# Kernel tuning notes

Measured on AMD Instinct MI355X. Metric: run time of the kernel, lower is better.

## Reference

```python
import jax, jax.numpy as jnp
import numpy as np

B, T, C = 8, 1024, 768
H, D = 12, 64

def setup_inputs() -> dict:
    key = jax.random.key(0)
    ks = jax.random.split(key, 6)
    s = 0.02
    return {
        "x": jax.random.normal(ks[0], (B, T, C), dtype=jnp.float32),
        "Wq": jax.random.normal(ks[1], (H, C, D), dtype=jnp.float32) * s,
        "Wk": jax.random.normal(ks[2], (H, C, D), dtype=jnp.float32) * s,
        "Wv": jax.random.normal(ks[3], (H, C, D), dtype=jnp.float32) * s,
        "Wproj": jax.random.normal(ks[4], (C, C), dtype=jnp.float32) * s,
        "bproj": jnp.zeros((C,), dtype=jnp.float32),
    }

def reference(x, Wq, Wk, Wv, Wproj, bproj):
    # per-head projections, vectorized over heads: [B,H,T,D]
    q = jnp.einsum('btc,hcd->bhtd', x, Wq)
    k = jnp.einsum('btc,hcd->bhtd', x, Wk)
    v = jnp.einsum('btc,hcd->bhtd', x, Wv)
    scale = 1.0 / jnp.sqrt(jnp.asarray(q.shape[-1], q.dtype))
    scores = jnp.einsum('bhtd,bhsd->bhts', q, k) * scale  # [B,H,T,T]
    attn = jax.nn.softmax(scores, axis=-1)
    out = jnp.einsum('bhts,bhsd->bhtd', attn, v)          # [B,H,T,D]
    # concat heads along last dim -> [B,T,H*D]
    out = out.transpose(0, 2, 1, 3).reshape(x.shape[0], x.shape[1], -1)
    return out @ Wproj + bproj
```

## Files before the change

### kernel.cpp

```cpp
#include <hip/hip_runtime.h>
#include <hip/hip_bf16.h>

using u16 = unsigned short;

typedef __attribute__((ext_vector_type(8))) short bf16x8;
typedef __attribute__((ext_vector_type(4))) float f32x4;
typedef __attribute__((ext_vector_type(16))) float f32x16;

#define B_ 8
#define T_ 1024
#define C_ 768
#define H_ 12
#define D_ 64

typedef const void __attribute__((address_space(1))) gv_t;
typedef void __attribute__((address_space(3))) lv_t;

__device__ __forceinline__ void gload_lds16(const void* g, void* l) {
  __builtin_amdgcn_global_load_lds((gv_t*)g, (lv_t*)l, 16, 0, 0);
}

__device__ __forceinline__ u16 f2b(float f) {
  union { float f; unsigned u; } a; a.f = f;
  unsigned r = a.u + 0x7FFFu + ((a.u >> 16) & 1u);
  return (u16)(r >> 16);
}

__device__ __forceinline__ float fexp2(float x) {
  float r;
  asm("v_exp_f32 %0, %1" : "=v"(r) : "v"(x));
  return r;
}

__device__ __forceinline__ unsigned cvtpk_bf16(float lo, float hi) {
  unsigned r;
  asm("v_cvt_pk_bf16_f32 %0, %1, %2" : "=v"(r) : "v"(lo), "v"(hi));
  return r;
}
__device__ __forceinline__ void plane32_swap(unsigned &a, unsigned &b) {
  asm volatile("v_permlane32_swap_b32 %0, %1" : "+v"(a), "+v"(b));
}

__global__ __launch_bounds__(256) void prep_all(
    const float* __restrict__ x,
    const float* __restrict__ Wq, const float* __restrict__ Wk,
    const float* __restrict__ Wv, const float* __restrict__ Wp,
    u16* __restrict__ Xb, u16* __restrict__ Wqkvt, u16* __restrict__ Wpt)
{
  int bb = blockIdx.x;
  if (bb < 3072) {
    int i = (bb * 256 + threadIdx.x) * 8;
    float4 a = *(const float4*)(x + i);
    float4 b = *(const float4*)(x + i + 4);
    union { bf16x8 v; u16 s[8]; } o;
    o.s[0] = f2b(a.x); o.s[1] = f2b(a.y); o.s[2] = f2b(a.z); o.s[3] = f2b(a.w);
    o.s[4] = f2b(b.x); o.s[5] = f2b(b.y); o.s[6] = f2b(b.z); o.s[7] = f2b(b.w);
    *(bf16x8*)(Xb + i) = o.v;
  } else {
    int idx = (bb - 3072) * 256 + threadIdx.x;
    int p = idx / 147456;
    int r = idx - p * 147456;
    if (p < 3) {
      const float* W = (p == 0) ? Wq : ((p == 1) ? Wk : Wv);
      int d4 = r & 15;
      int c  = (r >> 4) % 768;
      int h  = r / 12288;
      float4 v = *(const float4*)(W + (size_t)h * 49152 + (size_t)c * 64 + d4 * 4);
      size_t nb = (size_t)p * 589824 + ((size_t)h * 64 + d4 * 4) * 768 + c;
      Wqkvt[nb]           = f2b(v.x);
      Wqkvt[nb + 768]     = f2b(v.y);
      Wqkvt[nb + 1536]    = f2b(v.z);
      Wqkvt[nb + 2304]    = f2b(v.w);
    } else {
      int co4 = r % 192;
      int ci  = r / 192;
      float4 v = *(const float4*)(Wp + (size_t)ci * 768 + co4 * 4);
      size_t ob = (size_t)(co4 * 4) * 768 + ci;
      Wpt[ob]        = f2b(v.x);
      Wpt[ob + 768]  = f2b(v.y);
      Wpt[ob + 1536] = f2b(v.z);
      Wpt[ob + 2304] = f2b(v.w);
    }
  }
}

__global__ __launch_bounds__(512) void gemm_qkv(
    const u16* __restrict__ X, const u16* __restrict__ Wt,
    u16* __restrict__ Qw, u16* __restrict__ Kw, u16* __restrict__ Vt)
{
  __shared__ __align__(16) u16 As[256 * 64];
  __shared__ __align__(16) u16 Bs[128 * 64];
  const int t = threadIdx.x;
  const int l = t & 63, w = t >> 6;
  const int lr = l & 15;
  const int hc = (l >> 4) * 16;
  const int m0 = blockIdx.x * 256;
  const int n0 = blockIdx.y * 128;
  const int wr = (w >> 1) * 64;
  const int wc = (w & 1) * 64;

  f32x4 acc[4][4] = {};

  for (int k0 = 0; k0 < 768; k0 += 64) {
    #pragma unroll
    for (int q = 0; q < 4; ++q) {
      int db = q * 8192 + t * 16;
      int row = db >> 7;
      int cb = (db ^ ((row & 7) << 4)) & 127;
      gload_lds16((const char*)X + ((size_t)(m0 + row) * 768 + k0) * 2 + cb,
                  (char*)As + db);
    }
    #pragma unroll
    for (int q = 0; q < 2; ++q) {
      int db = q * 8192 + t * 16;
      int row = db >> 7;
      int cb = (db ^ ((row & 7) << 4)) & 127;
      gload_lds16((const char*)Wt + ((size_t)(n0 + row) * 768 + k0) * 2 + cb,
                  (char*)Bs + db);
    }
    asm volatile("s_waitcnt vmcnt(0)" ::: "memory");
    __syncthreads();
    #pragma unroll
    for (int kq = 0; kq < 2; ++kq) {
      bf16x8 af[4], bfr[4];
      #pragma unroll
      for (int i = 0; i < 4; ++i) {
        int ra = wr + i * 16 + lr;
        int Ua = ra * 128 + kq * 64 + hc;
        af[i] = *(const bf16x8*)((const char*)As + (Ua ^ ((ra & 7) << 4)));
        int rb = wc + i * 16 + lr;
        int Ub = rb * 128 + kq * 64 + hc;
        bfr[i] = *(const bf16x8*)((const char*)Bs + (Ub ^ ((rb & 7) << 4)));
      }
      #pragma unroll
      for (int i = 0; i < 4; ++i)
        #pragma unroll
        for (int j = 0; j < 4; ++j)
          acc[i][j] = __builtin_amdgcn_mfma_f32_16x16x32_bf16(af[i], bfr[j],
                                                              acc[i][j], 0, 0, 0);
    }
    __syncthreads();
  }

  #pragma unroll
  for (int j = 0; j < 4; ++j) {
    int col_g = n0 + wc + j * 16 + lr;
    int p = (col_g >= 1536) ? 2 : ((col_g >= 768) ? 1 : 0);
    int rr = col_g - p * 768;
    int h = rr >> 6, d = rr & 63;
    #pragma unroll
    for (int i = 0; i < 4; ++i) {
      int rg0 = m0 + wr + i * 16 + ((l >> 4) << 2);
      int b = rg0 >> 10, tt = rg0 & 1023;
      if (p == 0) {
        size_t base = (((size_t)b * H_ + h) * T_ + tt) * D_ + d;
        #pragma unroll
        for (int r = 0; r < 4; ++r)
          Qw[base + (size_t)r * D_] = f2b(acc[i][j][r] * 0.18033688f);
      } else if (p == 1) {
        size_t base = (((size_t)b * H_ + h) * T_ + tt) * D_ + d;
        #pragma unroll
        for (int r = 0; r < 4; ++r) Kw[base + (size_t)r * D_] = f2b(acc[i][j][r]);
      } else {
        unsigned long long pk =
            (unsigned long long)f2b(acc[i][j][0]) |
            ((unsigned long long)f2b(acc[i][j][1]) << 16) |
            ((unsigned long long)f2b(acc[i][j][2]) << 32) |
            ((unsigned long long)f2b(acc[i][j][3]) << 48);
        *reinterpret_cast<unsigned long long*>(
            &Vt[(((size_t)b * H_ + h) * D_ + d) * T_ + tt]) = pk;
      }
    }
  }
}

__global__ __launch_bounds__(256) void gemm_proj(
    const u16* __restrict__ A, const u16* __restrict__ Wt,
    const float* __restrict__ bias, float* __restrict__ O)
{
  __shared__ __align__(16) u16 As[128 * 64];
  __shared__ __align__(16) u16 Bs[128 * 64];
  const int t = threadIdx.x;
  const int l = t & 63, w = t >> 6;
  const int lr = l & 15;
  const int hc = (l >> 4) * 16;
  const int m0 = blockIdx.x * 128;
  const int n0 = blockIdx.y * 128;
  const int wr = (w >> 1) * 64, wc = (w & 1) * 64;

  f32x4 acc[4][4] = {};
  for (int k0 = 0; k0 < 768; k0 += 64) {
    #pragma unroll
    for (int q = 0; q < 4; ++q) {
      int db = q * 4096 + t * 16;
      int row = db >> 7;
      int cb = (db ^ ((row & 7) << 4)) & 127;
      gload_lds16((const char*)A + ((size_t)(m0 + row) * 768 + k0) * 2 + cb,
                  (char*)As + db);
      gload_lds16((const char*)Wt + ((size_t)(n0 + row) * 768 + k0) * 2 + cb,
                  (char*)Bs + db);
    }
    asm volatile("s_waitcnt vmcnt(0)" ::: "memory");
    __syncthreads();
    #pragma unroll
    for (int kq = 0; kq < 2; ++kq) {
      bf16x8 af[4], bfr[4];
      #pragma unroll
      for (int i = 0; i < 4; ++i) {
        int ra = wr + i * 16 + lr;
        int Ua = ra * 128 + kq * 64 + hc;
        af[i] = *(const bf16x8*)((const char*)As + (Ua ^ ((ra & 7) << 4)));
        int rb = wc + i * 16 + lr;
        int Ub = rb * 128 + kq * 64 + hc;
        bfr[i] = *(const bf16x8*)((const char*)Bs + (Ub ^ ((rb & 7) << 4)));
      }
      #pragma unroll
      for (int i = 0; i < 4; ++i)
        #pragma unroll
        for (int j = 0; j < 4; ++j)
          acc[i][j] = __builtin_amdgcn_mfma_f32_16x16x32_bf16(af[i], bfr[j],
                                                              acc[i][j], 0, 0, 0);
    }
    __syncthreads();
  }

  #pragma unroll
  for (int j = 0; j < 4; ++j) {
    int col_g = n0 + wc + j * 16 + lr;
    float bb = bias[col_g];
    #pragma unroll
    for (int i = 0; i < 4; ++i) {
      int rg0 = m0 + wr + i * 16 + ((l >> 4) << 2);
      #pragma unroll
      for (int r = 0; r < 4; ++r)
        O[(size_t)(rg0 + r) * C_ + col_g] = acc[i][j][r] + bb;
    }
  }
}

__global__ __launch_bounds__(256) void attn_fwd(
    const u16* __restrict__ Qw, const u16* __restrict__ Kw,
    const u16* __restrict__ VT, u16* __restrict__ AO)
{
  __shared__ __align__(16) u16 Ks[2][64 * 64];
  __shared__ __align__(16) u16 Vs[3][64 * 64];
  const int t = threadIdx.x, l = t & 63;
  const int lq = l & 31, lh = l >> 5;

  const int bid = blockIdx.x;
  const int bh = (bid & 7) * 12 + ((bid >> 3) >> 3);
  const int qt = (bid >> 3) & 7;
  const int b = bh / H_, h = bh - b * H_;
  const u16* Qh = Qw + (size_t)bh * (T_ * D_);
  const char* Kp = (const char*)(Kw + (size_t)bh * (T_ * D_));
  const char* Vp = (const char*)(VT + (size_t)bh * (D_ * T_));
  const int q0w = qt * 128 + (t >> 6) * 32;
  const int qrow = q0w + lq;

  bf16x8 qf[4];
  #pragma unroll
  for (int ks = 0; ks < 4; ++ks)
    qf[ks] = *(const bf16x8*)(Qh + (size_t)qrow * D_ + lh * 8 + ks * 16);

  bf16x8 ones;
  {
    union { u16 s[8]; bf16x8 v; } u;
    #pragma unroll
    for (int j = 0; j < 8; ++j) u.s[j] = 0x3F80;
    ones = u.v;
  }

  f32x16 oA = {}, oB = {}, lacc = {};
  bf16x8 pbP[4];

  const int db0 = t * 16, db1 = 4096 + t * 16;
  const int row0 = db0 >> 7, row1 = db1 >> 7;
  const int cb0 = (db0 ^ ((row0 & 7) << 4)) & 127;
  const int cb1 = (db1 ^ ((row1 & 7) << 4)) & 127;

#define ISSUE_TILE(KT, KB, VB)                                                   \
  gload_lds16(Kp + (size_t)((KT) + row0) * 128 + cb0, (char*)Ks[KB] + db0);      \
  gload_lds16(Kp + (size_t)((KT) + row1) * 128 + cb1, (char*)Ks[KB] + db1);      \
  gload_lds16(Vp + (size_t)row0 * 2048 + (KT) * 2 + cb0, (char*)Vs[VB] + db0);   \
  gload_lds16(Vp + (size_t)row1 * 2048 + (KT) * 2 + cb1, (char*)Vs[VB] + db1);

  ISSUE_TILE(0, 0, 0)

  int wv = 1, pv = 2;

  for (int kt_i = 0; kt_i < 16; ++kt_i) {
    const int cur = kt_i & 1;
    asm volatile("s_waitcnt vmcnt(0)" ::: "memory");
    __syncthreads();
    if (kt_i < 15) { ISSUE_TILE((kt_i + 1) * 64, cur ^ 1, wv) }

    f32x16 sA = {}, sB = {};
    {
      bf16x8 ka[4];
      #pragma unroll
      for (int ks = 0; ks < 4; ++ks) {
        int row = lq;
        int U = row * 128 + ks * 32 + lh * 16;
        ka[ks] = *(const bf16x8*)((const char*)Ks[cur] + (U ^ ((row & 7) << 4)));
      }
      #pragma unroll
      for (int ks = 0; ks < 4; ++ks)
        sA = __builtin_amdgcn_mfma_f32_32x32x16_bf16(ka[ks], qf[ks], sA, 0, 0, 0);
      #pragma unroll
      for (int ks = 0; ks < 4; ++ks) {
        int row = lq + 32;
        int U = row * 128 + ks * 32 + lh * 16;
        ka[ks] = *(const bf16x8*)((const char*)Ks[cur] + (U ^ ((row & 7) << 4)));
      }
      #pragma unroll
      for (int ks = 0; ks < 4; ++ks)
        sB = __builtin_amdgcn_mfma_f32_32x32x16_bf16(ka[ks], qf[ks], sB, 0, 0, 0);
    }

    if (kt_i > 0) {
      const char* Vb = (const char*)Vs[pv];
      bf16x8 va[4];
      #pragma unroll
      for (int ks = 0; ks < 4; ++ks) {
        int row = lq;
        int U = row * 128 + ks * 32 + lh * 16;
        va[ks] = *(const bf16x8*)(Vb + (U ^ ((row & 7) << 4)));
      }
      #pragma unroll
      for (int ks = 0; ks < 4; ++ks)
        oA = __builtin_amdgcn_mfma_f32_32x32x16_bf16(va[ks], pbP[ks], oA, 0, 0, 0);
      #pragma unroll
      for (int ks = 0; ks < 4; ++ks) {
        int row = lq + 32;
        int U = row * 128 + ks * 32 + lh * 16;
        va[ks] = *(const bf16x8*)(Vb + (U ^ ((row & 7) << 4)));
      }
      #pragma unroll
      for (int ks = 0; ks < 4; ++ks)
        oB = __builtin_amdgcn_mfma_f32_32x32x16_bf16(va[ks], pbP[ks], oB, 0, 0, 0);
      #pragma unroll
      for (int ks = 0; ks < 4; ++ks)
        lacc = __builtin_amdgcn_mfma_f32_32x32x16_bf16(ones, pbP[ks], lacc, 0, 0, 0);
    }

    #pragma unroll
    for (int r = 0; r < 16; ++r) {
      sA[r] = fexp2(sA[r]);
      sB[r] = fexp2(sB[r]);
    }

    #pragma unroll
    for (int ks = 0; ks < 4; ++ks) {
      f32x16& S = (ks < 2) ? sA : sB;
      const int g = (ks & 1) * 8;
      unsigned a0 = cvtpk_bf16(S[g + 0], S[g + 1]);
      unsigned a1 = cvtpk_bf16(S[g + 2], S[g + 3]);
      unsigned b0 = cvtpk_bf16(S[g + 4], S[g + 5]);
      unsigned b1 = cvtpk_bf16(S[g + 6], S[g + 7]);
      plane32_swap(a0, b0);
      plane32_swap(a1, b1);
      union { unsigned wd[4]; bf16x8 v; } u;
      u.wd[0] = a0; u.wd[1] = a1; u.wd[2] = b0; u.wd[3] = b1;
      pbP[ks] = u.v;
    }

    wv = (wv == 2) ? 0 : wv + 1;
    pv = (pv == 2) ? 0 : pv + 1;
  }
#undef ISSUE_TILE

  {
    const char* Vb = (const char*)Vs[pv];
    bf16x8 va[4];
    #pragma unroll
    for (int ks = 0; ks < 4; ++ks) {
      int row = lq;
      int U = row * 128 + ks * 32 + lh * 16;
      va[ks] = *(const bf16x8*)(Vb + (U ^ ((row & 7) << 4)));
    }
    #pragma unroll
    for (int ks = 0; ks < 4; ++ks)
      oA = __builtin_amdgcn_mfma_f32_32x32x16_bf16(va[ks], pbP[ks], oA, 0, 0, 0);
    #pragma unroll
    for (int ks = 0; ks < 4; ++ks) {
      int row = lq + 32;
      int U = row * 128 + ks * 32 + lh * 16;
      va[ks] = *(const bf16x8*)(Vb + (U ^ ((row & 7) << 4)));
    }
    #pragma unroll
    for (int ks = 0; ks < 4; ++ks)
      oB = __builtin_amdgcn_mfma_f32_32x32x16_bf16(va[ks], pbP[ks], oB, 0, 0, 0);
    #pragma unroll
    for (int ks = 0; ks < 4; ++ks)
      lacc = __builtin_amdgcn_mfma_f32_32x32x16_bf16(ones, pbP[ks], lacc, 0, 0, 0);
  }

  float inv = 1.0f / lacc[0];
  size_t base = ((size_t)b * T_ + qrow) * C_ + h * D_;
  #pragma unroll
  for (int dh = 0; dh < 2; ++dh) {
    const f32x16& OO = dh ? oB : oA;
    #pragma unroll
    for (int g = 0; g < 4; ++g) {
      int d0 = 8 * g + 4 * lh + 32 * dh;
      unsigned long long pk =
          (unsigned long long)f2b(OO[4 * g + 0] * inv) |
          ((unsigned long long)f2b(OO[4 * g + 1] * inv) << 16) |
          ((unsigned long long)f2b(OO[4 * g + 2] * inv) << 32) |
          ((unsigned long long)f2b(OO[4 * g + 3] * inv) << 48);
      *reinterpret_cast<unsigned long long*>(&AO[base + d0]) = pk;
    }
  }
}

extern "C" void kernel_launch(void* const* d_in, const int* in_sizes, int n_in,
                              void* d_out, int out_size, void* d_ws, size_t ws_size,
                              hipStream_t stream) {
  (void)in_sizes; (void)n_in; (void)out_size;
  const float* x     = (const float*)d_in[0];
  const float* Wq    = (const float*)d_in[1];
  const float* Wk    = (const float*)d_in[2];
  const float* Wv    = (const float*)d_in[3];
  const float* Wproj = (const float*)d_in[4];
  const float* bproj = (const float*)d_in[5];

  const size_t NEEDED = 55050240;
  if (ws_size < NEEDED) return;

  char* ws = (char*)d_ws;
  u16* Wpt   = (u16*)(ws);
  u16* Qw    = (u16*)(ws + 1179648);
  u16* Kw    = (u16*)(ws + 13762560);
  u16* Vt    = (u16*)(ws + 26345472);
  u16* Xb    = (u16*)(ws + 38928384);
  u16* AO    = (u16*)(ws + 38928384);
  u16* Wqkvt = (u16*)(ws + 51511296);

  prep_all<<<dim3(5376), dim3(256), 0, stream>>>(x, Wq, Wk, Wv, Wproj, Xb, Wqkvt, Wpt);
  gemm_qkv<<<dim3(32, 18), dim3(512), 0, stream>>>(Xb, Wqkvt, Qw, Kw, Vt);
  attn_fwd<<<dim3(768), dim3(256), 0, stream>>>(Qw, Kw, Vt, AO);
  gemm_proj<<<dim3(64, 6), dim3(256), 0, stream>>>(AO, Wpt, bproj, (float*)d_out);
}
```

Before: 127.9 us.

## Double-buffer LDS tiles in QKV GEMM to overlap global loads with MFMA

The QKV projection GEMM now keeps two LDS buffers for the A and B tiles. It issues the next k-tile's global-to-LDS loads, split across the two k-halves, while MFMAs run on the current buffer, and it drops the trailing barrier. This aims to hide global load latency behind compute. In exchange, LDS use doubles to 96KB per block, which may limit occupancy, and only one barrier per iteration now guards buffer reuse.

```diff
diff --git a/kernel.cpp b/kernel.cpp
--- a/kernel.cpp
+++ b/kernel.cpp
@@ -88,8 +88,8 @@
     const u16* __restrict__ X, const u16* __restrict__ Wt,
     u16* __restrict__ Qw, u16* __restrict__ Kw, u16* __restrict__ Vt)
 {
-  __shared__ __align__(16) u16 As[256 * 64];
-  __shared__ __align__(16) u16 Bs[128 * 64];
+  __shared__ __align__(16) u16 As[2][256 * 64];
+  __shared__ __align__(16) u16 Bs[2][128 * 64];
   const int t = threadIdx.x;
   const int l = t & 63, w = t >> 6;
   const int lr = l & 15;
@@ -99,38 +99,45 @@
   const int wr = (w >> 1) * 64;
   const int wc = (w & 1) * 64;
 
+#define QKV_ISSUE_A(K0, BUF)                                                    \
+  _Pragma("unroll")                                                             \
+  for (int q = 0; q < 4; ++q) {                                                 \
+    int db = q * 8192 + t * 16;                                                 \
+    int row = db >> 7;                                                          \
+    int cb = (db ^ ((row & 7) << 4)) & 127;                                     \
+    gload_lds16((const char*)X + ((size_t)(m0 + row) * 768 + (K0)) * 2 + cb,    \
+                (char*)As[BUF] + db);                                           \
+  }
+#define QKV_ISSUE_B(K0, BUF)                                                    \
+  _Pragma("unroll")                                                             \
+  for (int q = 0; q < 2; ++q) {                                                 \
+    int db = q * 8192 + t * 16;                                                 \
+    int row = db >> 7;                                                          \
+    int cb = (db ^ ((row & 7) << 4)) & 127;                                     \
+    gload_lds16((const char*)Wt + ((size_t)(n0 + row) * 768 + (K0)) * 2 + cb,   \
+                (char*)Bs[BUF] + db);                                           \
+  }
+
+  QKV_ISSUE_A(0, 0)
+  QKV_ISSUE_B(0, 0)
+
   f32x4 acc[4][4] = {};
-
-  for (int k0 = 0; k0 < 768; k0 += 64) {
-    #pragma unroll
-    for (int q = 0; q < 4; ++q) {
-      int db = q * 8192 + t * 16;
-      int row = db >> 7;
-      int cb = (db ^ ((row & 7) << 4)) & 127;
-      gload_lds16((const char*)X + ((size_t)(m0 + row) * 768 + k0) * 2 + cb,
-                  (char*)As + db);
-    }
-    #pragma unroll
-    for (int q = 0; q < 2; ++q) {
-      int db = q * 8192 + t * 16;
-      int row = db >> 7;
-      int cb = (db ^ ((row & 7) << 4)) & 127;
-      gload_lds16((const char*)Wt + ((size_t)(n0 + row) * 768 + k0) * 2 + cb,
-                  (char*)Bs + db);
-    }
+  for (int it = 0; it < 12; ++it) {
+    const int c = it & 1;
     asm volatile("s_waitcnt vmcnt(0)" ::: "memory");
     __syncthreads();
-    #pragma unroll
-    for (int kq = 0; kq < 2; ++kq) {
+    if (it < 11) { QKV_ISSUE_A((it + 1) * 64, c ^ 1) }
+
+    {
       bf16x8 af[4], bfr[4];
       #pragma unroll
       for (int i = 0; i < 4; ++i) {
         int ra = wr + i * 16 + lr;
-        int Ua = ra * 128 + kq * 64 + hc;
-        af[i] = *(const bf16x8*)((const char*)As + (Ua ^ ((ra & 7) << 4)));
+        int Ua = ra * 128 + hc;
+        af[i] = *(const bf16x8*)((const char*)As[c] + (Ua ^ ((ra & 7) << 4)));
         int rb = wc + i * 16 + lr;
-        int Ub = rb * 128 + kq * 64 + hc;
-        bfr[i] = *(const bf16x8*)((const char*)Bs + (Ub ^ ((rb & 7) << 4)));
+        int Ub = rb * 128 + hc;
+        bfr[i] = *(const bf16x8*)((const char*)Bs[c] + (Ub ^ ((rb & 7) << 4)));
       }
       #pragma unroll
       for (int i = 0; i < 4; ++i)
@@ -139,8 +146,30 @@
           acc[i][j] = __builtin_amdgcn_mfma_f32_16x16x32_bf16(af[i], bfr[j],
                                                               acc[i][j], 0, 0, 0);
     }
-    __syncthreads();
-  }
+
+    if (it < 11) { QKV_ISSUE_B((it + 1) * 64, c ^ 1) }
+
+    {
+      bf16x8 af[4], bfr[4];
+      #pragma unroll
+      for (int i = 0; i < 4; ++i) {
+        int ra = wr + i * 16 + lr;
+        int Ua = ra * 128 + 64 + hc;
+        af[i] = *(const bf16x8*)((const char*)As[c] + (Ua ^ ((ra & 7) << 4)));
+        int rb = wc + i * 16 + lr;
+        int Ub = rb * 128 + 64 + hc;
+        bfr[i] = *(const bf16x8*)((const char*)Bs[c] + (Ub ^ ((rb & 7) << 4)));
+      }
+      #pragma unroll
+      for (int i = 0; i < 4; ++i)
+        #pragma unroll
+        for (int j = 0; j < 4; ++j)
+          acc[i][j] = __builtin_amdgcn_mfma_f32_16x16x32_bf16(af[i], bfr[j],
+                                                              acc[i][j], 0, 0, 0);
+    }
+  }
+#undef QKV_ISSUE_A
+#undef QKV_ISSUE_B
 
   #pragma unroll
   for (int j = 0; j < 4; ++j) {
```

After: 138.3 us. +8.1%, slower.

## Replace LDS-tiled GEMMs with per-wave direct-global-load MFMA tiles

Applied to the files above, without the earlier changes.

Both the QKV and output-projection GEMMs drop shared-memory staging and block-wide barriers. Each wave now computes its own 64x64 output tile and loads the MFMA operands straight from global memory (through L2/L1) into registers. This removes the LDS round trip and the syncthreads stalls and raises occupancy, but gives up cross-wave data reuse in LDS and issues uncoalesced, strided 16-byte loads with no software prefetch, so the GEMMs depend on cache hit rates.

```diff
diff --git a/kernel.cpp b/kernel.cpp
--- a/kernel.cpp
+++ b/kernel.cpp
@@ -84,73 +84,49 @@
   }
 }
 
-__global__ __launch_bounds__(512) void gemm_qkv(
+__global__ __launch_bounds__(256, 4) void gemm_qkv(
     const u16* __restrict__ X, const u16* __restrict__ Wt,
     u16* __restrict__ Qw, u16* __restrict__ Kw, u16* __restrict__ Vt)
 {
-  __shared__ __align__(16) u16 As[256 * 64];
-  __shared__ __align__(16) u16 Bs[128 * 64];
   const int t = threadIdx.x;
   const int l = t & 63, w = t >> 6;
   const int lr = l & 15;
-  const int hc = (l >> 4) * 16;
-  const int m0 = blockIdx.x * 256;
-  const int n0 = blockIdx.y * 128;
-  const int wr = (w >> 1) * 64;
-  const int wc = (w & 1) * 64;
+  const int ko = (l >> 4) * 8;
+  const int gw = blockIdx.x * 4 + w;
+  const int mw = gw / 36, nw = gw - mw * 36;
+  const int m0 = mw * 64, n0 = nw * 64;
+
+  const u16* Xa = X  + (size_t)(m0 + lr) * 768 + ko;
+  const u16* Wa = Wt + (size_t)(n0 + lr) * 768 + ko;
 
   f32x4 acc[4][4] = {};
-
-  for (int k0 = 0; k0 < 768; k0 += 64) {
-    #pragma unroll
-    for (int q = 0; q < 4; ++q) {
-      int db = q * 8192 + t * 16;
-      int row = db >> 7;
-      int cb = (db ^ ((row & 7) << 4)) & 127;
-      gload_lds16((const char*)X + ((size_t)(m0 + row) * 768 + k0) * 2 + cb,
-                  (char*)As + db);
-    }
-    #pragma unroll
-    for (int q = 0; q < 2; ++q) {
-      int db = q * 8192 + t * 16;
-      int row = db >> 7;
-      int cb = (db ^ ((row & 7) << 4)) & 127;
-      gload_lds16((const char*)Wt + ((size_t)(n0 + row) * 768 + k0) * 2 + cb,
-                  (char*)Bs + db);
-    }
-    asm volatile("s_waitcnt vmcnt(0)" ::: "memory");
-    __syncthreads();
-    #pragma unroll
-    for (int kq = 0; kq < 2; ++kq) {
-      bf16x8 af[4], bfr[4];
-      #pragma unroll
-      for (int i = 0; i < 4; ++i) {
-        int ra = wr + i * 16 + lr;
-        int Ua = ra * 128 + kq * 64 + hc;
-        af[i] = *(const bf16x8*)((const char*)As + (Ua ^ ((ra & 7) << 4)));
-        int rb = wc + i * 16 + lr;
-        int Ub = rb * 128 + kq * 64 + hc;
-        bfr[i] = *(const bf16x8*)((const char*)Bs + (Ub ^ ((rb & 7) << 4)));
-      }
-      #pragma unroll
-      for (int i = 0; i < 4; ++i)
-        #pragma unroll
-        for (int j = 0; j < 4; ++j)
-          acc[i][j] = __builtin_amdgcn_mfma_f32_16x16x32_bf16(af[i], bfr[j],
-                                                              acc[i][j], 0, 0, 0);
-    }
-    __syncthreads();
+  #pragma unroll
+  for (int ks = 0; ks < 24; ++ks) {
+    const int kk = ks * 32;
+    bf16x8 af[4], bfr[4];
+    #pragma unroll
+    for (int i = 0; i < 4; ++i)
+      af[i] = *(const bf16x8*)(Xa + (size_t)i * (16 * 768) + kk);
+    #pragma unroll
+    for (int j = 0; j < 4; ++j)
+      bfr[j] = *(const bf16x8*)(Wa + (size_t)j * (16 * 768) + kk);
+    #pragma unroll
+    for (int i = 0; i < 4; ++i)
+      #pragma unroll
+      for (int j = 0; j < 4; ++j)
+        acc[i][j] = __builtin_amdgcn_mfma_f32_16x16x32_bf16(af[i], bfr[j],
+                                                            acc[i][j], 0, 0, 0);
   }
 
   #pragma unroll
   for (int j = 0; j < 4; ++j) {
-    int col_g = n0 + wc + j * 16 + lr;
+    int col_g = n0 + j * 16 + lr;
     int p = (col_g >= 1536) ? 2 : ((col_g >= 768) ? 1 : 0);
     int rr = col_g - p * 768;
     int h = rr >> 6, d = rr & 63;
     #pragma unroll
     for (int i = 0; i < 4; ++i) {
-      int rg0 = m0 + wr + i * 16 + ((l >> 4) << 2);
+      int rg0 = m0 + i * 16 + ((l >> 4) << 2);
       int b = rg0 >> 10, tt = rg0 & 1023;
       if (p == 0) {
         size_t base = (((size_t)b * H_ + h) * T_ + tt) * D_ + d;
@@ -174,63 +150,47 @@
   }
 }
 
-__global__ __launch_bounds__(256) void gemm_proj(
+__global__ __launch_bounds__(256, 4) void gemm_proj(
     const u16* __restrict__ A, const u16* __restrict__ Wt,
     const float* __restrict__ bias, float* __restrict__ O)
 {
-  __shared__ __align__(16) u16 As[128 * 64];
-  __shared__ __align__(16) u16 Bs[128 * 64];
   const int t = threadIdx.x;
   const int l = t & 63, w = t >> 6;
   const int lr = l & 15;
-  const int hc = (l >> 4) * 16;
-  const int m0 = blockIdx.x * 128;
-  const int n0 = blockIdx.y * 128;
-  const int wr = (w >> 1) * 64, wc = (w & 1) * 64;
+  const int ko = (l >> 4) * 8;
+  const int gw = blockIdx.x * 4 + w;
+  const int mw = gw / 12, nw = gw - mw * 12;
+  const int m0 = mw * 64, n0 = nw * 64;
+
+  const u16* Aa = A  + (size_t)(m0 + lr) * 768 + ko;
+  const u16* Wa = Wt + (size_t)(n0 + lr) * 768 + ko;
 
   f32x4 acc[4][4] = {};
-  for (int k0 = 0; k0 < 768; k0 += 64) {
-    #pragma unroll
-    for (int q = 0; q < 4; ++q) {
-      int db = q * 4096 + t * 16;
-      int row = db >> 7;
-      int cb = (db ^ ((row & 7) << 4)) & 127;
-      gload_lds16((const char*)A + ((size_t)(m0 + row) * 768 + k0) * 2 + cb,
-                  (char*)As + db);
-      gload_lds16((const char*)Wt + ((size_t)(n0 + row) * 768 + k0) * 2 + cb,
-                  (char*)Bs + db);
-    }
-    asm volatile("s_waitcnt vmcnt(0)" ::: "memory");
-    __syncthreads();
-    #pragma unroll
-    for (int kq = 0; kq < 2; ++kq) {
-      bf16x8 af[4], bfr[4];
-      #pragma unroll
-      for (int i = 0; i < 4; ++i) {
-        int ra = wr + i * 16 + lr;
-        int Ua = ra * 128 + kq * 64 + hc;
-        af[i] = *(const bf16x8*)((const char*)As + (Ua ^ ((ra & 7) << 4)));
-        int rb = wc + i * 16 + lr;
-        int Ub = rb * 128 + kq * 64 + hc;
-        bfr[i] = *(const bf16x8*)((const char*)Bs + (Ub ^ ((rb & 7) << 4)));
-      }
-      #pragma unroll
-      for (int i = 0; i < 4; ++i)
-        #pragma unroll
-        for (int j = 0; j < 4; ++j)
-          acc[i][j] = __builtin_amdgcn_mfma_f32_16x16x32_bf16(af[i], bfr[j],
-                                                              acc[i][j], 0, 0, 0);
-    }
-    __syncthreads();
+  #pragma unroll
+  for (int ks = 0; ks < 24; ++ks) {
+    const int kk = ks * 32;
+    bf16x8 af[4], bfr[4];
+    #pragma unroll
+    for (int i = 0; i < 4; ++i)
+      af[i] = *(const bf16x8*)(Aa + (size_t)i * (16 * 768) + kk);
+    #pragma unroll
+    for (int j = 0; j < 4; ++j)
+      bfr[j] = *(const bf16x8*)(Wa + (size_t)j * (16 * 768) + kk);
+    #pragma unroll
+    for (int i = 0; i < 4; ++i)
+      #pragma unroll
+      for (int j = 0; j < 4; ++j)
+        acc[i][j] = __builtin_amdgcn_mfma_f32_16x16x32_bf16(af[i], bfr[j],
+                                                            acc[i][j], 0, 0, 0);
   }
 
   #pragma unroll
   for (int j = 0; j < 4; ++j) {
-    int col_g = n0 + wc + j * 16 + lr;
+    int col_g = n0 + j * 16 + lr;
     float bb = bias[col_g];
     #pragma unroll
     for (int i = 0; i < 4; ++i) {
-      int rg0 = m0 + wr + i * 16 + ((l >> 4) << 2);
+      int rg0 = m0 + i * 16 + ((l >> 4) << 2);
       #pragma unroll
       for (int r = 0; r < 4; ++r)
         O[(size_t)(rg0 + r) * C_ + col_g] = acc[i][j][r] + bb;
@@ -437,7 +397,7 @@
   u16* Wqkvt = (u16*)(ws + 51511296);
 
   prep_all<<<dim3(5376), dim3(256), 0, stream>>>(x, Wq, Wk, Wv, Wproj, Xb, Wqkvt, Wpt);
-  gemm_qkv<<<dim3(32, 18), dim3(512), 0, stream>>>(Xb, Wqkvt, Qw, Kw, Vt);
+  gemm_qkv<<<dim3(1152), dim3(256), 0, stream>>>(Xb, Wqkvt, Qw, Kw, Vt);
   attn_fwd<<<dim3(768), dim3(256), 0, stream>>>(Qw, Kw, Vt, AO);
-  gemm_proj<<<dim3(64, 6), dim3(256), 0, stream>>>(AO, Wpt, bproj, (float*)d_out);
-}
+  gemm_proj<<<dim3(384), dim3(256), 0, stream>>>(AO, Wpt, bproj, (float*)d_out);
+}
```

After: 231.7 us. +81.1%, slower.
